# Kernel tuning notes

Hardware: AMD Instinct MI355X
Metric: run time of the kernel (lower is better)

## Reference

```python
import jax, jax.numpy as jnp
import numpy as np

PROJ_DIM = 8192
INPUT_DIM = 512
THRESH = 1e-08


def _signed_sqrt(x):
    return jnp.sign(x) * jnp.sqrt(jnp.abs(x))


def _make_sketch_matrix(key, input_dim, proj_dim):
    kh, ks = jax.random.split(key)
    h = jax.random.randint(kh, (input_dim,), 0, proj_dim)
    s = jnp.sign(jax.random.uniform(ks, (input_dim,), minval=-1.0, maxval=1.0)).astype(jnp.float32)
    M = jnp.zeros((input_dim, proj_dim), dtype=jnp.float32)
    return M.at[jnp.arange(input_dim), h].set(s)


def setup_inputs() -> dict:
    key = jax.random.key(0)
    kx, k1, k2 = jax.random.split(key, 3)
    x = jax.random.normal(kx, (32, 14, 14, INPUT_DIM), dtype=jnp.float32)
    M1 = _make_sketch_matrix(k1, INPUT_DIM, PROJ_DIM)
    M2 = _make_sketch_matrix(k2, INPUT_DIM, PROJ_DIM)
    return {"x": x, "M1": M1, "M2": M2}


def reference(x, M1, M2):
    B, H, W, C = x.shape
    x_flat = x.reshape(-1, C)                      # [B*H*W, C]
    # count-sketch projections (dense matmul, as in the original layer)
    p1 = (x_flat @ M1).astype(jnp.complex64)       # [B*H*W, P]
    p2 = (x_flat @ M2).astype(jnp.complex64)
    # circular convolution via FFT
    sketch = jnp.fft.fft(p1, axis=-1) * jnp.fft.fft(p2, axis=-1)
    y = jnp.real(jnp.fft.ifft(sketch, axis=-1)).astype(jnp.float32)
    y = y.reshape(B, H, W, -1).sum(axis=(1, 2))    # sum-pool over spatial dims -> [B, P]
    y = _signed_sqrt(y)
    # tf.nn.l2_normalize(x, axis=1, epsilon=1e-10)
    inv_norm = jax.lax.rsqrt(jnp.maximum(jnp.sum(y * y, axis=1, keepdims=True), 1e-10))
    return y * inv_norm
```

## Files before the change

kernel.cpp:

```cpp
#include <hip/hip_runtime.h>
#include <math.h>

#define PROJ 8192
#define CDIM 512
#define HWPOS 196
#define NBATCH 32
#define NSLAB 7
#define NSEG 16

typedef __attribute__((ext_vector_type(8))) short   short8;
typedef __attribute__((ext_vector_type(4))) float   f32x4;

__device__ __forceinline__ unsigned short f2bf(float f) {
    unsigned u = __float_as_uint(f);
    u += 0x7fff + ((u >> 16) & 1);
    return (unsigned short)(u >> 16);
}
__device__ __forceinline__ float bf2f(unsigned short h) {
    return __uint_as_float(((unsigned)h) << 16);
}

__device__ __forceinline__ void lds_uadd(unsigned* p, unsigned v) {
    __attribute__((address_space(3))) unsigned* lp =
        (__attribute__((address_space(3))) unsigned*)p;
    asm volatile("ds_add_u32 %0, %1" : : "v"(lp), "v"(v) : "memory");
}
__device__ __forceinline__ unsigned lds_uadd_rtn(unsigned* p, unsigned v) {
    __attribute__((address_space(3))) unsigned* lp =
        (__attribute__((address_space(3))) unsigned*)p;
    unsigned r;
    asm volatile("ds_add_rtn_u32 %0, %1, %2\n\ts_waitcnt lgkmcnt(0)"
                 : "=v"(r) : "v"(lp), "v"(v) : "memory");
    return r;
}

#define BI_PACK 0x2110002110003210ULL
#define BJ_PACK 0x3323213323213210ULL

__device__ __forceinline__ void seg_entry(int seg, int e,
    const int* __restrict__ h1, const float* __restrict__ s1,
    const int* __restrict__ h2, const float* __restrict__ s2,
    int& bin, int& sg)
{
    const int bi = (int)((BI_PACK >> (seg * 4)) & 15);
    const int bj = (int)((BJ_PACK >> (seg * 4)) & 15);
    const int r = e >> 7, c = e & 127;
    int gi, gj;
    if (seg < 10) { gi = bi * 128 + r; gj = bj * 128 + c; }
    else          { gi = bj * 128 + c; gj = bi * 128 + r; }
    bin = (h1[gi] + h2[gj]) & (PROJ - 1);
    sg  = (int)((__float_as_uint(s1[gi]) ^ __float_as_uint(s2[gj])) >> 31);
}

__global__ __launch_bounds__(256) void extract_kernel(
    const float* __restrict__ M1, const float* __restrict__ M2,
    int* __restrict__ h1, float* __restrict__ s1,
    int* __restrict__ h2, float* __restrict__ s2,
    float* __restrict__ norm)
{
    const int row = blockIdx.x;
    const float* M = blockIdx.y ? M2 : M1;
    int*   h = blockIdx.y ? h2 : h1;
    float* s = blockIdx.y ? s2 : s1;
    const float* mrow = M + (size_t)row * PROJ;

    if (blockIdx.x == 0 && blockIdx.y == 0 && threadIdx.x < NBATCH)
        norm[threadIdx.x] = 0.0f;

    for (int i = threadIdx.x * 4; i < PROJ; i += 256 * 4) {
        float4 v = *(const float4*)(mrow + i);
        if (v.x != 0.0f) { h[row] = i + 0; s[row] = v.x; }
        if (v.y != 0.0f) { h[row] = i + 1; s[row] = v.y; }
        if (v.z != 0.0f) { h[row] = i + 2; s[row] = v.z; }
        if (v.w != 0.0f) { h[row] = i + 3; s[row] = v.w; }
    }
}

__global__ __launch_bounds__(256) void combo_kernel(
    const float* __restrict__ x,
    unsigned short* __restrict__ XThi, unsigned short* __restrict__ XTlo,
    const int* __restrict__ h1, const float* __restrict__ s1,
    const int* __restrict__ h2, const float* __restrict__ s2,
    unsigned* __restrict__ csr)
{
    __shared__ float    xt[32][513];
    __shared__ unsigned cnt[PROJ];
    __shared__ unsigned sc[256];
    const int tid = threadIdx.x;

    if (blockIdx.x < 224) {
        const int ks = blockIdx.x % NSLAB;
        const int bt = blockIdx.x / NSLAB;
        const float* xb = x + (size_t)bt * HWPOS * CDIM;
        const int k0 = ks * 32;
#pragma unroll
        for (int i = 0; i < 16; ++i) {
            const int idx = i * 1024 + tid * 4;
            const int kr  = idx >> 9;
            const int c   = idx & 511;
            float4 v = make_float4(0.f, 0.f, 0.f, 0.f);
            if (k0 + kr < HWPOS) v = *(const float4*)(xb + (size_t)(k0 + kr) * CDIM + c);
            xt[kr][c+0] = v.x; xt[kr][c+1] = v.y; xt[kr][c+2] = v.z; xt[kr][c+3] = v.w;
        }
        __syncthreads();

        unsigned short* ohi = XThi + ((size_t)bt * NSLAB + ks) * 16384;
        unsigned short* olo = XTlo + ((size_t)bt * NSLAB + ks) * 16384;
#pragma unroll
        for (int i = 0; i < 8; ++i) {
            const int ch   = i * 256 + tid;
            const int c16  = ch & 15;
            const int quad = (ch >> 4) & 3;
            const int cgrp = ch >> 6;
            const int c    = cgrp * 16 + c16;
            short8 vh, vl;
#pragma unroll
            for (int j = 0; j < 8; ++j) {
                float f = xt[quad * 8 + j][c];
                unsigned short h = f2bf(f);
                vh[j] = (short)h;
                vl[j] = (short)f2bf(f - bf2f(h));
            }
            *(short8*)(ohi + ch * 8) = vh;
            *(short8*)(olo + ch * 8) = vl;
        }
    } else {
        const int seg = blockIdx.x - 224;

        for (int i = tid; i < PROJ; i += 256) cnt[i] = 0u;
        __syncthreads();
#pragma unroll 8
        for (int k = 0; k < 64; ++k) {
            const int e = k * 256 + tid;
            int bin, sg;
            seg_entry(seg, e, h1, s1, h2, s2, bin, sg);
            lds_uadd(&cnt[bin], 1u);
        }
        __syncthreads();

        unsigned c[32]; unsigned tot = 0;
#pragma unroll
        for (int i = 0; i < 32; ++i) { c[i] = cnt[tid * 32 + i]; tot += c[i]; }
        sc[tid] = tot;
        __syncthreads();
        for (int off = 1; off < 256; off <<= 1) {
            unsigned v = (tid >= off) ? sc[tid - off] : 0u;
            __syncthreads();
            sc[tid] += v;
            __syncthreads();
        }
        unsigned base = sc[tid] - tot;
#pragma unroll
        for (int i = 0; i < 32; ++i) { unsigned t = c[i]; cnt[tid * 32 + i] = base; base += t; }
        __syncthreads();

        unsigned* cs = csr + (size_t)seg * 16384;
#pragma unroll 8
        for (int k = 0; k < 64; ++k) {
            const int e = k * 256 + tid;
            int bin, sg;
            seg_entry(seg, e, h1, s1, h2, s2, bin, sg);
            const unsigned pos = lds_uadd_rtn(&cnt[bin], 1u);
            cs[pos] = ((unsigned)bin << 15) | ((unsigned)sg << 14) | (unsigned)e;
        }
    }
}

__global__ __launch_bounds__(256) void gramgather_kernel(
    const unsigned short* __restrict__ XThi, const unsigned short* __restrict__ XTlo,
    const unsigned* __restrict__ csr, float* __restrict__ pbins)
{
    const int id  = blockIdx.x;
    const int sub = id >> 3;
    const int tp  = sub & 15;
    const int bat = (id & 7) + 8 * (sub >> 4);
    const int bi = (int)((BI_PACK >> (tp * 4)) & 15);
    const int bj = (int)((BJ_PACK >> (tp * 4)) & 15);

    const int tid  = threadIdx.x;
    const int w    = tid >> 6;
    const int lane = tid & 63;
    const int rowq = w >> 1, colq = w & 1;

    __shared__ __align__(16) unsigned short Sbuf[2][4][4096];

    const int tile = (w < 2) ? bi : bj;
    const unsigned short* srcbase = ((w & 1) ? XTlo : XThi)
                                  + (size_t)bat * NSLAB * 16384 + (size_t)tile * 4096;

    {
        const unsigned short* src = srcbase;
        unsigned short* dst = &Sbuf[0][w][0];
#pragma unroll
        for (int i = 0; i < 8; ++i)
            __builtin_amdgcn_global_load_lds(
                (const __attribute__((address_space(1))) void*)(src + i * 512 + lane * 8),
                (__attribute__((address_space(3))) void*)(dst + i * 512), 16, 0, 0);
    }

    float* page = pbins + ((size_t)bat * NSEG + tp) * PROJ;
    for (int i = tid * 4; i < PROJ; i += 1024)
        *(float4*)(page + i) = make_float4(0.f, 0.f, 0.f, 0.f);

    f32x4 acc[16];
#pragma unroll
    for (int i = 0; i < 16; ++i) { acc[i][0]=0.f; acc[i][1]=0.f; acc[i][2]=0.f; acc[i][3]=0.f; }

    for (int ks = 0; ks < NSLAB; ++ks) {
        __syncthreads();
        const int buf = ks & 1;

        if (ks + 1 < NSLAB) {
            const unsigned short* src = srcbase + (size_t)(ks + 1) * 16384;
            unsigned short* dst = &Sbuf[buf ^ 1][w][0];
#pragma unroll
            for (int i = 0; i < 8; ++i)
                __builtin_amdgcn_global_load_lds(
                    (const __attribute__((address_space(1))) void*)(src + i * 512 + lane * 8),
                    (__attribute__((address_space(3))) void*)(dst + i * 512), 16, 0, 0);
        }

        short8 ah[4], al[4], bh4[4], bl[4];
#pragma unroll
        for (int t = 0; t < 4; ++t) {
            ah[t]  = *(const short8*)&Sbuf[buf][0][(rowq * 4 + t) * 512 + lane * 8];
            al[t]  = *(const short8*)&Sbuf[buf][1][(rowq * 4 + t) * 512 + lane * 8];
            bh4[t] = *(const short8*)&Sbuf[buf][2][(colq * 4 + t) * 512 + lane * 8];
            bl[t]  = *(const short8*)&Sbuf[buf][3][(colq * 4 + t) * 512 + lane * 8];
        }
#pragma unroll
        for (int mt = 0; mt < 4; ++mt)
#pragma unroll
            for (int nt = 0; nt < 4; ++nt) {
                const int idx = mt * 4 + nt;
                acc[idx] = __builtin_amdgcn_mfma_f32_16x16x32_bf16(ah[mt], bh4[nt], acc[idx], 0, 0, 0);
                acc[idx] = __builtin_amdgcn_mfma_f32_16x16x32_bf16(ah[mt], bl[nt],  acc[idx], 0, 0, 0);
                acc[idx] = __builtin_amdgcn_mfma_f32_16x16x32_bf16(al[mt], bh4[nt], acc[idx], 0, 0, 0);
            }
    }

    __syncthreads();
    float* tileL = (float*)Sbuf;
    const int quad = lane >> 4;
#pragma unroll
    for (int mt = 0; mt < 4; ++mt)
#pragma unroll
        for (int reg = 0; reg < 4; ++reg) {
            const int rl = rowq * 64 + mt * 16 + quad * 4 + reg;
#pragma unroll
            for (int nt = 0; nt < 4; ++nt) {
                const int cl = colq * 64 + nt * 16 + (lane & 15);
                tileL[rl * 128 + cl] = acc[mt * 4 + nt][reg];
            }
        }
    __syncthreads();

    const uint4* ce = (const uint4*)(csr + (size_t)tp * 16384 + (size_t)tid * 64);
    uint4 E[16];
#pragma unroll
    for (int i = 0; i < 16; ++i) E[i] = ce[i];

    float a = 0.f;
    unsigned cur = E[0].x >> 15;
    bool first = true;
#pragma unroll
    for (int i = 0; i < 16; ++i) {
#pragma unroll
        for (int j = 0; j < 4; ++j) {
            const unsigned ent = (j == 0) ? E[i].x : (j == 1) ? E[i].y
                               : (j == 2) ? E[i].z : E[i].w;
            const unsigned b = ent >> 15;
            float v = tileL[ent & 0x3FFF];
            v = (ent & 0x4000u) ? -v : v;
            if (b != cur) {
                if (first) { unsafeAtomicAdd(&page[cur], a); first = false; }
                else       { page[cur] = a; }
                cur = b; a = v;
            } else {
                a += v;
            }
        }
    }
    unsafeAtomicAdd(&page[cur], a);
}

__global__ __launch_bounds__(256) void reduce_kernel(
    const float* __restrict__ pbins, float* __restrict__ out,
    float* __restrict__ norm)
{
    const int chunk = blockIdx.x;
    const int bat   = blockIdx.y;
    const int tid   = threadIdx.x;
    const int base  = chunk * 1024 + tid * 4;

    const float* pb = pbins + (size_t)bat * NSEG * PROJ;
    float4 v = make_float4(0.f, 0.f, 0.f, 0.f);
#pragma unroll
    for (int t = 0; t < NSEG; ++t) {
        float4 p = *(const float4*)(pb + (size_t)t * PROJ + base);
        v.x += p.x; v.y += p.y; v.z += p.z; v.w += p.w;
    }

    float4 sv;
    sv.x = (v.x >= 0.f) ? sqrtf(v.x) : -sqrtf(-v.x);
    sv.y = (v.y >= 0.f) ? sqrtf(v.y) : -sqrtf(-v.y);
    sv.z = (v.z >= 0.f) ? sqrtf(v.z) : -sqrtf(-v.z);
    sv.w = (v.w >= 0.f) ? sqrtf(v.w) : -sqrtf(-v.w);
    *(float4*)(out + (size_t)bat * PROJ + base) = sv;

    float local = fabsf(v.x) + fabsf(v.y) + fabsf(v.z) + fabsf(v.w);
#pragma unroll
    for (int off = 32; off > 0; off >>= 1) local += __shfl_down(local, off, 64);

    __shared__ float wred[4];
    if ((tid & 63) == 0) wred[tid >> 6] = local;
    __syncthreads();
    if (tid == 0)
        unsafeAtomicAdd(&norm[bat], wred[0] + wred[1] + wred[2] + wred[3]);
}

__global__ __launch_bounds__(256) void normalize_kernel(
    float* __restrict__ out, const float* __restrict__ norm)
{
    const int bat = blockIdx.y;
    const int idx = blockIdx.x * 1024 + threadIdx.x * 4;
    const float inv = rsqrtf(fmaxf(norm[bat], 1e-10f));
    float4* p = (float4*)(out + (size_t)bat * PROJ + idx);
    float4 v = *p;
    v.x *= inv; v.y *= inv; v.z *= inv; v.w *= inv;
    *p = v;
}

extern "C" void kernel_launch(void* const* d_in, const int* in_sizes, int n_in,
                              void* d_out, int out_size, void* d_ws, size_t ws_size,
                              hipStream_t stream)
{
    const float* x  = (const float*)d_in[0];
    const float* M1 = (const float*)d_in[1];
    const float* M2 = (const float*)d_in[2];
    float* out = (float*)d_out;

    char* ws = (char*)d_ws;
    int*            h1    = (int*)   (ws + 0);
    float*          s1    = (float*) (ws + 2048);
    int*            h2    = (int*)   (ws + 4096);
    float*          s2    = (float*) (ws + 6144);
    float*          norm  = (float*) (ws + 8192);
    unsigned*       csr   = (unsigned*)(ws + 16384);
    unsigned short* XThi  = (unsigned short*)(ws + 1064960);
    unsigned short* XTlo  = (unsigned short*)(ws + 8404992);
    float*          pbins = (float*) (ws + 15745024);

    extract_kernel<<<dim3(512, 2), 256, 0, stream>>>(M1, M2, h1, s1, h2, s2, norm);
    combo_kernel<<<240, 256, 0, stream>>>(x, XThi, XTlo, h1, s1, h2, s2, csr);
    gramgather_kernel<<<NSEG * NBATCH, 256, 0, stream>>>(XThi, XTlo, csr, pbins);
    reduce_kernel<<<dim3(8, NBATCH), 256, 0, stream>>>(pbins, out, norm);
    normalize_kernel<<<dim3(8, NBATCH), 256, 0, stream>>>(out, norm);
}
```

Before: 162.2 us.

## Split combo kernel into prep and build; move pbins zeroing into extract

The fused combo kernel is split back into a separate x-transpose/bf16-split kernel (launched first, independent of extract) and a small CSR build kernel of 16 blocks. Zeroing of the partial-bin buffer moves from the gram-gather kernel into the extract kernel, where each of its 1024 blocks clears 4096 floats. The aim is to take the zeroing stores off the critical gram-gather kernel and give the heavy CSR blocks a kernel of their own. In exchange it adds one more kernel launch, and the 16-block build kernel now runs serially with no other work beside it.

Result: slower. 178.3 us (+9.9%).

```diff
diff --git a/kernel.cpp b/kernel.cpp
--- a/kernel.cpp
+++ b/kernel.cpp
@@ -52,11 +52,55 @@
     sg  = (int)((__float_as_uint(s1[gi]) ^ __float_as_uint(s2[gj])) >> 31);
 }
 
+__global__ __launch_bounds__(256) void prep_kernel(
+    const float* __restrict__ x,
+    unsigned short* __restrict__ XThi, unsigned short* __restrict__ XTlo)
+{
+    const int ks  = blockIdx.x;
+    const int bat = blockIdx.y;
+    const int tid = threadIdx.x;
+    __shared__ float xt[32][513];
+
+    const float* xb = x + (size_t)bat * HWPOS * CDIM;
+    const int k0 = ks * 32;
+#pragma unroll
+    for (int i = 0; i < 16; ++i) {
+        const int idx = i * 1024 + tid * 4;
+        const int kr  = idx >> 9;
+        const int c   = idx & 511;
+        float4 v = make_float4(0.f, 0.f, 0.f, 0.f);
+        if (k0 + kr < HWPOS) v = *(const float4*)(xb + (size_t)(k0 + kr) * CDIM + c);
+        xt[kr][c+0] = v.x; xt[kr][c+1] = v.y; xt[kr][c+2] = v.z; xt[kr][c+3] = v.w;
+    }
+    __syncthreads();
+
+    unsigned short* ohi = XThi + ((size_t)bat * NSLAB + ks) * 16384;
+    unsigned short* olo = XTlo + ((size_t)bat * NSLAB + ks) * 16384;
+#pragma unroll
+    for (int i = 0; i < 8; ++i) {
+        const int ch   = i * 256 + tid;
+        const int c16  = ch & 15;
+        const int quad = (ch >> 4) & 3;
+        const int cgrp = ch >> 6;
+        const int c    = cgrp * 16 + c16;
+        short8 vh, vl;
+#pragma unroll
+        for (int j = 0; j < 8; ++j) {
+            float f = xt[quad * 8 + j][c];
+            unsigned short h = f2bf(f);
+            vh[j] = (short)h;
+            vl[j] = (short)f2bf(f - bf2f(h));
+        }
+        *(short8*)(ohi + ch * 8) = vh;
+        *(short8*)(olo + ch * 8) = vl;
+    }
+}
+
 __global__ __launch_bounds__(256) void extract_kernel(
     const float* __restrict__ M1, const float* __restrict__ M2,
     int* __restrict__ h1, float* __restrict__ s1,
     int* __restrict__ h2, float* __restrict__ s2,
-    float* __restrict__ norm)
+    float* __restrict__ norm, float* __restrict__ pbins)
 {
     const int row = blockIdx.x;
     const float* M = blockIdx.y ? M2 : M1;
@@ -74,95 +118,59 @@
         if (v.z != 0.0f) { h[row] = i + 2; s[row] = v.z; }
         if (v.w != 0.0f) { h[row] = i + 3; s[row] = v.w; }
     }
-}
-
-__global__ __launch_bounds__(256) void combo_kernel(
-    const float* __restrict__ x,
-    unsigned short* __restrict__ XThi, unsigned short* __restrict__ XTlo,
+
+    const int bid = blockIdx.x * 2 + blockIdx.y;
+    float* pz = pbins + (size_t)bid * 4096;
+#pragma unroll
+    for (int i = 0; i < 4; ++i)
+        *(float4*)(pz + i * 1024 + threadIdx.x * 4) = make_float4(0.f, 0.f, 0.f, 0.f);
+}
+
+__global__ __launch_bounds__(256) void build_kernel(
     const int* __restrict__ h1, const float* __restrict__ s1,
     const int* __restrict__ h2, const float* __restrict__ s2,
     unsigned* __restrict__ csr)
 {
-    __shared__ float    xt[32][513];
     __shared__ unsigned cnt[PROJ];
     __shared__ unsigned sc[256];
     const int tid = threadIdx.x;
-
-    if (blockIdx.x < 224) {
-        const int ks = blockIdx.x % NSLAB;
-        const int bt = blockIdx.x / NSLAB;
-        const float* xb = x + (size_t)bt * HWPOS * CDIM;
-        const int k0 = ks * 32;
-#pragma unroll
-        for (int i = 0; i < 16; ++i) {
-            const int idx = i * 1024 + tid * 4;
-            const int kr  = idx >> 9;
-            const int c   = idx & 511;
-            float4 v = make_float4(0.f, 0.f, 0.f, 0.f);
-            if (k0 + kr < HWPOS) v = *(const float4*)(xb + (size_t)(k0 + kr) * CDIM + c);
-            xt[kr][c+0] = v.x; xt[kr][c+1] = v.y; xt[kr][c+2] = v.z; xt[kr][c+3] = v.w;
-        }
+    const int seg = blockIdx.x;
+
+    for (int i = tid; i < PROJ; i += 256) cnt[i] = 0u;
+    __syncthreads();
+#pragma unroll 8
+    for (int k = 0; k < 64; ++k) {
+        const int e = k * 256 + tid;
+        int bin, sg;
+        seg_entry(seg, e, h1, s1, h2, s2, bin, sg);
+        lds_uadd(&cnt[bin], 1u);
+    }
+    __syncthreads();
+
+    unsigned c[32]; unsigned tot = 0;
+#pragma unroll
+    for (int i = 0; i < 32; ++i) { c[i] = cnt[tid * 32 + i]; tot += c[i]; }
+    sc[tid] = tot;
+    __syncthreads();
+    for (int off = 1; off < 256; off <<= 1) {
+        unsigned v = (tid >= off) ? sc[tid - off] : 0u;
         __syncthreads();
-
-        unsigned short* ohi = XThi + ((size_t)bt * NSLAB + ks) * 16384;
-        unsigned short* olo = XTlo + ((size_t)bt * NSLAB + ks) * 16384;
-#pragma unroll
-        for (int i = 0; i < 8; ++i) {
-            const int ch   = i * 256 + tid;
-            const int c16  = ch & 15;
-            const int quad = (ch >> 4) & 3;
-            const int cgrp = ch >> 6;
-            const int c    = cgrp * 16 + c16;
-            short8 vh, vl;
-#pragma unroll
-            for (int j = 0; j < 8; ++j) {
-                float f = xt[quad * 8 + j][c];
-                unsigned short h = f2bf(f);
-                vh[j] = (short)h;
-                vl[j] = (short)f2bf(f - bf2f(h));
-            }
-            *(short8*)(ohi + ch * 8) = vh;
-            *(short8*)(olo + ch * 8) = vl;
-        }
-    } else {
-        const int seg = blockIdx.x - 224;
-
-        for (int i = tid; i < PROJ; i += 256) cnt[i] = 0u;
+        sc[tid] += v;
         __syncthreads();
+    }
+    unsigned base = sc[tid] - tot;
+#pragma unroll
+    for (int i = 0; i < 32; ++i) { unsigned t = c[i]; cnt[tid * 32 + i] = base; base += t; }
+    __syncthreads();
+
+    unsigned* cs = csr + (size_t)seg * 16384;
 #pragma unroll 8
-        for (int k = 0; k < 64; ++k) {
-            const int e = k * 256 + tid;
-            int bin, sg;
-            seg_entry(seg, e, h1, s1, h2, s2, bin, sg);
-            lds_uadd(&cnt[bin], 1u);
-        }
-        __syncthreads();
-
-        unsigned c[32]; unsigned tot = 0;
-#pragma unroll
-        for (int i = 0; i < 32; ++i) { c[i] = cnt[tid * 32 + i]; tot += c[i]; }
-        sc[tid] = tot;
-        __syncthreads();
-        for (int off = 1; off < 256; off <<= 1) {
-            unsigned v = (tid >= off) ? sc[tid - off] : 0u;
-            __syncthreads();
-            sc[tid] += v;
-            __syncthreads();
-        }
-        unsigned base = sc[tid] - tot;
-#pragma unroll
-        for (int i = 0; i < 32; ++i) { unsigned t = c[i]; cnt[tid * 32 + i] = base; base += t; }
-        __syncthreads();
-
-        unsigned* cs = csr + (size_t)seg * 16384;
-#pragma unroll 8
-        for (int k = 0; k < 64; ++k) {
-            const int e = k * 256 + tid;
-            int bin, sg;
-            seg_entry(seg, e, h1, s1, h2, s2, bin, sg);
-            const unsigned pos = lds_uadd_rtn(&cnt[bin], 1u);
-            cs[pos] = ((unsigned)bin << 15) | ((unsigned)sg << 14) | (unsigned)e;
-        }
+    for (int k = 0; k < 64; ++k) {
+        const int e = k * 256 + tid;
+        int bin, sg;
+        seg_entry(seg, e, h1, s1, h2, s2, bin, sg);
+        const unsigned pos = lds_uadd_rtn(&cnt[bin], 1u);
+        cs[pos] = ((unsigned)bin << 15) | ((unsigned)sg << 14) | (unsigned)e;
     }
 }
 
@@ -199,8 +207,6 @@
     }
 
     float* page = pbins + ((size_t)bat * NSEG + tp) * PROJ;
-    for (int i = tid * 4; i < PROJ; i += 1024)
-        *(float4*)(page + i) = make_float4(0.f, 0.f, 0.f, 0.f);
 
     f32x4 acc[16];
 #pragma unroll
@@ -351,8 +357,9 @@
     unsigned short* XTlo  = (unsigned short*)(ws + 8404992);
     float*          pbins = (float*) (ws + 15745024);
 
-    extract_kernel<<<dim3(512, 2), 256, 0, stream>>>(M1, M2, h1, s1, h2, s2, norm);
-    combo_kernel<<<240, 256, 0, stream>>>(x, XThi, XTlo, h1, s1, h2, s2, csr);
+    prep_kernel<<<dim3(NSLAB, NBATCH), 256, 0, stream>>>(x, XThi, XTlo);
+    extract_kernel<<<dim3(512, 2), 256, 0, stream>>>(M1, M2, h1, s1, h2, s2, norm, pbins);
+    build_kernel<<<NSEG, 256, 0, stream>>>(h1, s1, h2, s2, csr);
     gramgather_kernel<<<NSEG * NBATCH, 256, 0, stream>>>(XThi, XTlo, csr, pbins);
     reduce_kernel<<<dim3(8, NBATCH), 256, 0, stream>>>(pbins, out, norm);
     normalize_kernel<<<dim3(8, NBATCH), 256, 0, stream>>>(out, norm);
```
